# Optimization experiments

Hardware: AMD Instinct MI355X
Metric: run time of the kernel (lower is better)

## Reference

```python
import jax, jax.numpy as jnp
import numpy as np

N = 20000
E = 320000
IN_DIM = 128
HIDDEN = 256
HEADS = 4
HD = HIDDEN // HEADS  # 64 per-head channels in layer 1
OUT_DIM = 128
NEG_SLOPE = 0.2
BN_EPS = 1e-5


def setup_inputs() -> dict:
    key = jax.random.key(0)
    ks = jax.random.split(key, 16)
    inp = {
        "x": jax.random.normal(ks[0], (N, IN_DIM), dtype=jnp.float32),
        "edge_index": jax.random.randint(ks[1], (2, E), 0, N, dtype=jnp.int64),
        # layer 1: GATConv(IN_DIM, HD, heads=HEADS, concat=True)
        "W1": jax.random.normal(ks[2], (IN_DIM, HEADS * HD), dtype=jnp.float32) * (1.0 / np.sqrt(IN_DIM)),
        "att_src1": jax.random.normal(ks[3], (HEADS, HD), dtype=jnp.float32) * 0.1,
        "att_dst1": jax.random.normal(ks[4], (HEADS, HD), dtype=jnp.float32) * 0.1,
        "bias1": jnp.zeros((HEADS * HD,), dtype=jnp.float32),
        "bn1_gamma": jnp.ones((HIDDEN,), dtype=jnp.float32),
        "bn1_beta": jnp.zeros((HIDDEN,), dtype=jnp.float32),
        # layer 2: GATConv(HIDDEN, OUT_DIM, heads=1, concat=False)
        "W2": jax.random.normal(ks[5], (HIDDEN, OUT_DIM), dtype=jnp.float32) * (1.0 / np.sqrt(HIDDEN)),
        "att_src2": jax.random.normal(ks[6], (1, OUT_DIM), dtype=jnp.float32) * 0.1,
        "att_dst2": jax.random.normal(ks[7], (1, OUT_DIM), dtype=jnp.float32) * 0.1,
        "bias2": jnp.zeros((OUT_DIM,), dtype=jnp.float32),
        "bn2_gamma": jnp.ones((OUT_DIM,), dtype=jnp.float32),
        "bn2_beta": jnp.zeros((OUT_DIM,), dtype=jnp.float32),
    }
    return inp


def _gat_conv(x, src, dst, W, a_src, a_dst, bias, heads, concat):
    """PyG GATConv with add_self_loops=True (self-loops already in src/dst)."""
    n = x.shape[0]
    hd = W.shape[1] // heads
    h = (x @ W).reshape(n, heads, hd)                     # [N, H, hd]
    alpha_s = jnp.einsum('nhd,hd->nh', h, a_src)          # [N, H]
    alpha_d = jnp.einsum('nhd,hd->nh', h, a_dst)          # [N, H]
    e = alpha_s[src] + alpha_d[dst]                       # [Etot, H]
    e = jnp.where(e > 0, e, NEG_SLOPE * e)                # leaky_relu
    # edge-softmax over incoming edges of each destination node
    m = jax.ops.segment_max(e, dst, num_segments=n)       # [N, H]
    ex = jnp.exp(e - m[dst])
    denom = jax.ops.segment_sum(ex, dst, num_segments=n)  # [N, H]
    alpha = ex / (denom[dst] + 1e-16)                     # [Etot, H]
    msg = h[src] * alpha[..., None]                       # [Etot, H, hd]
    out = jax.ops.segment_sum(msg, dst, num_segments=n)   # [N, H, hd]
    if concat:
        out = out.reshape(n, heads * hd)
    else:
        out = out.mean(axis=1)
    return out + bias


def _batch_norm(x, gamma, beta):
    mean = x.mean(axis=0)
    var = ((x - mean) ** 2).mean(axis=0)  # biased, training-mode BN
    return (x - mean) * jax.lax.rsqrt(var + BN_EPS) * gamma + beta


def reference(x, edge_index, W1, att_src1, att_dst1, bias1, bn1_gamma, bn1_beta,
              W2, att_src2, att_dst2, bias2, bn2_gamma, bn2_beta):
    n = x.shape[0]
    loop = jnp.arange(n, dtype=edge_index.dtype)
    src = jnp.concatenate([edge_index[0], loop])  # add self-loops (PyG default)
    dst = jnp.concatenate([edge_index[1], loop])

    h = _gat_conv(x, src, dst, W1, att_src1, att_dst1, bias1, HEADS, True)
    h = _batch_norm(h, bn1_gamma, bn1_beta)
    h = jax.nn.elu(h)

    h = _gat_conv(h, src, dst, W2, att_src2, att_dst2, bias2, 1, False)
    h = _batch_norm(h, bn2_gamma, bn2_beta)
    return h
```

## Files before the change

kernel.cpp:

```cpp
#include <hip/hip_runtime.h>
#include <type_traits>

constexpr int N_N  = 20000;
constexpr int N_E  = 320000;
constexpr int N_ET = N_E + N_N;
constexpr int IN_D = 128;
constexpr int HID  = 256;
constexpr int H1   = 4;
constexpr int OUTD = 128;
constexpr float SLOPE = 0.2f;
constexpr float BNEPS = 1e-5f;
constexpr int NPART = 32;

typedef unsigned short u16;
typedef float f32x4 __attribute__((ext_vector_type(4)));
typedef short bf16x8 __attribute__((ext_vector_type(8)));

__device__ __forceinline__ float bf2f(u16 u) { return __uint_as_float((unsigned)u << 16); }
__device__ __forceinline__ u16 f2bf(float f) {
  unsigned u = __float_as_uint(f);
  unsigned r = u + 0x7FFFu + ((u >> 16) & 1u);
  return (u16)(r >> 16);
}

__global__ __launch_bounds__(256) void prep_k(const int* __restrict__ ei,
                                              const float* __restrict__ W1,
                                              const float* __restrict__ W2,
                                              u16* __restrict__ wp1,
                                              u16* __restrict__ wp2,
                                              int* __restrict__ cnt) {
  const int i = blockIdx.x * 256 + threadIdx.x;
  if (i < IN_D * HID) {
    const int n = i >> 7, k = i & 127;
    wp1[i] = f2bf(W1[(size_t)k * HID + n]);
  }
  if (i < HID * OUTD) {
    const int n = i >> 8, k = i & 255;
    wp2[i] = f2bf(W2[(size_t)k * OUTD + n]);
  }
  if (i < N_ET) {
    const int dst = (i < N_E) ? ei[N_E + i] : (i - N_E);
    atomicAdd(&cnt[dst], 1);
  }
}

__global__ __launch_bounds__(1024) void scan_k(const int* __restrict__ cnt,
                                               int* __restrict__ rowptr,
                                               int* __restrict__ wcur) {
  __shared__ int wsum[17];
  const int tid = threadIdx.x, lane = tid & 63, wv = tid >> 6;
  constexpr int CHK = 20;
  const int base = tid * CHK;
  int c[CHK];
  int s = 0;
#pragma unroll
  for (int j = 0; j < CHK; ++j) {
    const int idx = base + j;
    c[j] = (idx < N_N) ? cnt[idx] : 0;
    s += c[j];
  }
  const int own = s;
#pragma unroll
  for (int off = 1; off < 64; off <<= 1) {
    const int v = __shfl_up(s, off, 64);
    if (lane >= off) s += v;
  }
  if (lane == 63) wsum[wv] = s;
  __syncthreads();
  if (tid == 0) {
    int run = 0;
#pragma unroll
    for (int i = 0; i < 16; ++i) { const int t = wsum[i]; wsum[i] = run; run += t; }
    wsum[16] = run;
  }
  __syncthreads();
  int run = wsum[wv] + (s - own);
#pragma unroll
  for (int j = 0; j < CHK; ++j) {
    const int idx = base + j;
    if (idx < N_N) {
      rowptr[idx] = run;
      wcur[idx]   = run;
      run += c[j];
    }
  }
  if (tid == 0) rowptr[N_N] = wsum[16];
}

constexpr int GB1 = N_N / 16;
__global__ __launch_bounds__(256) void sg_k(const float* __restrict__ x,
                                            const u16* __restrict__ wp,
                                            const float* __restrict__ asrc,
                                            const float* __restrict__ adst,
                                            u16* __restrict__ h,
                                            float* __restrict__ as_,
                                            float* __restrict__ ad_,
                                            const int* __restrict__ ei,
                                            int* __restrict__ wcur,
                                            int* __restrict__ col) {
  const int tid = threadIdx.x;
  if (blockIdx.x >= GB1) {
    const int i = (blockIdx.x - GB1) * 256 + tid;
    if (i >= N_ET) return;
    int s, dst;
    if (i < N_E) { s = ei[i]; dst = ei[N_E + i]; } else { s = dst = i - N_E; }
    const int pos = atomicAdd(&wcur[dst], 1);
    col[pos] = s;
    return;
  }
  const int wv = tid >> 6, lane = tid & 63;
  const int q = lane >> 4, t = lane & 15;
  const int m0 = blockIdx.x * 16;
  const int n0 = wv * 64;
  f32x4 acc[4] = {};
#pragma unroll
  for (int kb = 0; kb < 4; ++kb) {
    const int k0 = kb * 32 + q * 8;
    const float4 x0 = *(const float4*)(x + (size_t)(m0 + t) * 128 + k0);
    const float4 x1 = *(const float4*)(x + (size_t)(m0 + t) * 128 + k0 + 4);
    bf16x8 a;
    a[0] = (short)f2bf(x0.x); a[1] = (short)f2bf(x0.y);
    a[2] = (short)f2bf(x0.z); a[3] = (short)f2bf(x0.w);
    a[4] = (short)f2bf(x1.x); a[5] = (short)f2bf(x1.y);
    a[6] = (short)f2bf(x1.z); a[7] = (short)f2bf(x1.w);
#pragma unroll
    for (int nt = 0; nt < 4; ++nt) {
      const int n = n0 + nt * 16 + t;
      const bf16x8 b = *(const bf16x8*)(wp + (size_t)n * 128 + k0);
      acc[nt] = __builtin_amdgcn_mfma_f32_16x16x32_bf16(a, b, acc[nt], 0, 0, 0);
    }
  }
  float ps[4] = {0.f, 0.f, 0.f, 0.f}, pd[4] = {0.f, 0.f, 0.f, 0.f};
#pragma unroll
  for (int nt = 0; nt < 4; ++nt) {
    const int coln = n0 + nt * 16 + t;
    const float a_s = asrc[coln], a_d = adst[coln];
#pragma unroll
    for (int r = 0; r < 4; ++r) {
      const float d = acc[nt][r];
      h[(size_t)(m0 + q * 4 + r) * 256 + coln] = f2bf(d);
      ps[r] += d * a_s;
      pd[r] += d * a_d;
    }
  }
#pragma unroll
  for (int off = 1; off < 16; off <<= 1)
#pragma unroll
    for (int r = 0; r < 4; ++r) {
      ps[r] += __shfl_xor(ps[r], off, 64);
      pd[r] += __shfl_xor(pd[r], off, 64);
    }
  if (t == 0) {
#pragma unroll
    for (int r = 0; r < 4; ++r) {
      const int row = m0 + q * 4 + r;
      as_[(size_t)row * 4 + wv] = ps[r];
      ad_[(size_t)row * 4 + wv] = pd[r];
    }
  }
}

__global__ __launch_bounds__(256) void gat_agg1_k(const int* __restrict__ rowptr,
                                                  const int* __restrict__ col,
                                                  const u16* __restrict__ h,
                                                  const float* __restrict__ as_,
                                                  const float* __restrict__ ad_,
                                                  u16* __restrict__ out,
                                                  float* __restrict__ accp) {
  __shared__ __align__(16) float s_w[4][64][4];
  __shared__ __align__(16) float st_s[4][256], st_q[4][256];
  const int tid = threadIdx.x;
  const int wv = tid >> 6, lane = tid & 63;
  const int n = blockIdx.x * 4 + wv;
  const int beg = rowptr[n], end = rowptr[n + 1];
  const int c0 = lane * 4;
  const int hl = lane >> 4;
  const float4 adv = *(const float4*)(ad_ + (size_t)n * 4);

  float a0 = 0.f, a1 = 0.f, a2 = 0.f, a3 = 0.f, smh = 0.f;

  for (int j0 = beg; j0 < end; j0 += 64) {
    const int cnt = min(64, end - j0);
    const int j = j0 + lane;
    const int sl = col[(j < end) ? j : beg];

    ushort4 gA[8];
#pragma unroll
    for (int u = 0; u < 8; ++u) {
      const int sv = __shfl(sl, u, 64);
      gA[u] = *(const ushort4*)(h + (size_t)sv * 256 + c0);
    }

    const float4 av = *(const float4*)(as_ + (size_t)sl * 4);
    float e0 = av.x + adv.x; e0 = e0 > 0.f ? e0 : SLOPE * e0;
    float e1 = av.y + adv.y; e1 = e1 > 0.f ? e1 : SLOPE * e1;
    float e2 = av.z + adv.z; e2 = e2 > 0.f ? e2 : SLOPE * e2;
    float e3 = av.w + adv.w; e3 = e3 > 0.f ? e3 : SLOPE * e3;
    const bool valid = j < end;
    float4 w4;
    w4.x = valid ? __expf(e0) : 0.f;
    w4.y = valid ? __expf(e1) : 0.f;
    w4.z = valid ? __expf(e2) : 0.f;
    w4.w = valid ? __expf(e3) : 0.f;
    *(float4*)(&s_w[wv][lane][0]) = w4;

    const int rounds = (cnt + 7) >> 3;
    for (int r = 0; r < rounds; ++r) {
      ushort4 gB[8];
      if (r + 1 < rounds) {
        const int nb = (r + 1) * 8;
#pragma unroll
        for (int u = 0; u < 8; ++u) {
          const int sv = __shfl(sl, nb + u, 64);
          gB[u] = *(const ushort4*)(h + (size_t)sv * 256 + c0);
        }
      }
      const int rb = r * 8;
#pragma unroll
      for (int u = 0; u < 8; ++u) {
        const float w = s_w[wv][rb + u][hl];
        smh += w;
        a0 = fmaf(w, bf2f(gA[u].x), a0);
        a1 = fmaf(w, bf2f(gA[u].y), a1);
        a2 = fmaf(w, bf2f(gA[u].z), a2);
        a3 = fmaf(w, bf2f(gA[u].w), a3);
      }
      if (r + 1 < rounds) {
#pragma unroll
        for (int u = 0; u < 8; ++u) gA[u] = gB[u];
      }
    }
  }

  const float rr = 1.f / (smh + 1e-16f);
  const float v0 = a0 * rr, v1 = a1 * rr, v2 = a2 * rr, v3 = a3 * rr;
  ushort4 o;
  o.x = f2bf(v0); o.y = f2bf(v1); o.z = f2bf(v2); o.w = f2bf(v3);
  *(ushort4*)(out + (size_t)n * 256 + c0) = o;

  float4 sv4, qv4;
  sv4.x = v0; sv4.y = v1; sv4.z = v2; sv4.w = v3;
  qv4.x = v0 * v0; qv4.y = v1 * v1; qv4.z = v2 * v2; qv4.w = v3 * v3;
  *(float4*)(&st_s[wv][c0]) = sv4;
  *(float4*)(&st_q[wv][c0]) = qv4;
  __syncthreads();
  {
    const int c = tid;
    const float s = st_s[0][c] + st_s[1][c] + st_s[2][c] + st_s[3][c];
    const float q = st_q[0][c] + st_q[1][c] + st_q[2][c] + st_q[3][c];
    float* dst = accp + (size_t)(blockIdx.x & (NPART - 1)) * 512;
    atomicAdd(&dst[c], s);
    atomicAdd(&dst[256 + c], q);
  }
}

__global__ __launch_bounds__(256) void gat_agg2_k(const int* __restrict__ rowptr,
                                                  const int* __restrict__ col,
                                                  const u16* __restrict__ h,
                                                  const float* __restrict__ as_,
                                                  const float* __restrict__ ad_,
                                                  u16* __restrict__ out,
                                                  float* __restrict__ accp) {
  __shared__ __align__(16) float st_s[4][128], st_q[4][128];
  const int tid = threadIdx.x;
  const int wv = tid >> 6, lane = tid & 63;
  const int n = blockIdx.x * 4 + wv;
  const int beg = rowptr[n], end = rowptr[n + 1];
  const int eh = lane >> 5;
  const int cl = (lane & 31) * 4;
  const float adv = ad_[n];

  float a0 = 0.f, a1 = 0.f, a2 = 0.f, a3 = 0.f, smh = 0.f;

  for (int j0 = beg; j0 < end; j0 += 64) {
    const int cnt = min(64, end - j0);
    const int j = j0 + lane;
    const int sl = col[(j < end) ? j : beg];
    float e = as_[sl] + adv;
    e = e > 0.f ? e : SLOPE * e;
    const float ew = (j < end) ? __expf(e) : 0.f;

    const int rounds = (cnt + 15) >> 4;
    ushort4 gA[8];
#pragma unroll
    for (int u = 0; u < 8; ++u) {
      const int es = u * 2 + eh;
      const int sv = __shfl(sl, es, 64);
      gA[u] = *(const ushort4*)(h + (size_t)sv * 128 + cl);
    }
    for (int r = 0; r < rounds; ++r) {
      ushort4 gB[8];
      if (r + 1 < rounds) {
        const int nb = (r + 1) * 16;
#pragma unroll
        for (int u = 0; u < 8; ++u) {
          const int es = nb + u * 2 + eh;
          const int sv = __shfl(sl, es, 64);
          gB[u] = *(const ushort4*)(h + (size_t)sv * 128 + cl);
        }
      }
      const int rb = r * 16;
#pragma unroll
      for (int u = 0; u < 8; ++u) {
        const float w = __shfl(ew, rb + u * 2 + eh, 64);
        smh += w;
        a0 = fmaf(w, bf2f(gA[u].x), a0);
        a1 = fmaf(w, bf2f(gA[u].y), a1);
        a2 = fmaf(w, bf2f(gA[u].z), a2);
        a3 = fmaf(w, bf2f(gA[u].w), a3);
      }
      if (r + 1 < rounds) {
#pragma unroll
        for (int u = 0; u < 8; ++u) gA[u] = gB[u];
      }
    }
  }

  a0 += __shfl_xor(a0, 32, 64);
  a1 += __shfl_xor(a1, 32, 64);
  a2 += __shfl_xor(a2, 32, 64);
  a3 += __shfl_xor(a3, 32, 64);
  smh += __shfl_xor(smh, 32, 64);

  const float rr = 1.f / (smh + 1e-16f);
  const float v0 = a0 * rr, v1 = a1 * rr, v2 = a2 * rr, v3 = a3 * rr;
  if (lane < 32) {
    ushort4 o;
    o.x = f2bf(v0); o.y = f2bf(v1); o.z = f2bf(v2); o.w = f2bf(v3);
    *(ushort4*)(out + (size_t)n * 128 + cl) = o;
    float4 sv4, qv4;
    sv4.x = v0; sv4.y = v1; sv4.z = v2; sv4.w = v3;
    qv4.x = v0 * v0; qv4.y = v1 * v1; qv4.z = v2 * v2; qv4.w = v3 * v3;
    *(float4*)(&st_s[wv][cl]) = sv4;
    *(float4*)(&st_q[wv][cl]) = qv4;
  }
  __syncthreads();
  if (tid < 128) {
    const int c = tid;
    const float s = st_s[0][c] + st_s[1][c] + st_s[2][c] + st_s[3][c];
    const float q = st_q[0][c] + st_q[1][c] + st_q[2][c] + st_q[3][c];
    float* dst = accp + (size_t)(blockIdx.x & (NPART - 1)) * 256;
    atomicAdd(&dst[c], s);
    atomicAdd(&dst[128 + c], q);
  }
}

__global__ __launch_bounds__(256) void gemm2_mfma_k(const u16* __restrict__ hin,
                                                    const float* __restrict__ accp,
                                                    const float* __restrict__ g1,
                                                    const float* __restrict__ b1,
                                                    const u16* __restrict__ wp,
                                                    const float* __restrict__ asrc,
                                                    const float* __restrict__ adst,
                                                    u16* __restrict__ h2,
                                                    float* __restrict__ as_,
                                                    float* __restrict__ ad_) {
  __shared__ float scsh[512];
  __shared__ float red[2][32][2];
  const int tid = threadIdx.x;
  {
    float s = 0.f, q = 0.f;
#pragma unroll
    for (int p = 0; p < NPART; ++p) {
      s += accp[(size_t)p * 512 + tid];
      q += accp[(size_t)p * 512 + 256 + tid];
    }
    const float mean = s * (1.f / N_N);
    const float var  = q * (1.f / N_N) - mean * mean;
    const float inv  = rsqrtf(var + BNEPS);
    const float sc   = g1[tid] * inv;
    scsh[tid]       = sc;
    scsh[256 + tid] = b1[tid] - mean * sc;
  }
  __syncthreads();
  const int wv = tid >> 6, lane = tid & 63;
  const int q = lane >> 4, t = lane & 15;
  const int mh = wv >> 1, nh = wv & 1;
  const int m0 = blockIdx.x * 32 + mh * 16;
  const int n0 = nh * 64;
  f32x4 acc[4] = {};
#pragma unroll
  for (int kb = 0; kb < 8; ++kb) {
    const int k0 = kb * 32 + q * 8;
    const ushort4 u0 = *(const ushort4*)(hin + (size_t)(m0 + t) * 256 + k0);
    const ushort4 u1 = *(const ushort4*)(hin + (size_t)(m0 + t) * 256 + k0 + 4);
    const float4 sc0 = *(const float4*)(scsh + k0);
    const float4 sc1 = *(const float4*)(scsh + k0 + 4);
    const float4 sh0 = *(const float4*)(scsh + 256 + k0);
    const float4 sh1 = *(const float4*)(scsh + 256 + k0 + 4);
    float v[8];
    v[0] = bf2f(u0.x) * sc0.x + sh0.x;
    v[1] = bf2f(u0.y) * sc0.y + sh0.y;
    v[2] = bf2f(u0.z) * sc0.z + sh0.z;
    v[3] = bf2f(u0.w) * sc0.w + sh0.w;
    v[4] = bf2f(u1.x) * sc1.x + sh1.x;
    v[5] = bf2f(u1.y) * sc1.y + sh1.y;
    v[6] = bf2f(u1.z) * sc1.z + sh1.z;
    v[7] = bf2f(u1.w) * sc1.w + sh1.w;
    bf16x8 a;
#pragma unroll
    for (int j = 0; j < 8; ++j) {
      const float e = v[j] > 0.f ? v[j] : __expf(v[j]) - 1.f;
      a[j] = (short)f2bf(e);
    }
#pragma unroll
    for (int nt = 0; nt < 4; ++nt) {
      const int n = n0 + nt * 16 + t;
      const bf16x8 b = *(const bf16x8*)(wp + (size_t)n * 256 + k0);
      acc[nt] = __builtin_amdgcn_mfma_f32_16x16x32_bf16(a, b, acc[nt], 0, 0, 0);
    }
  }
  float ps[4] = {0.f, 0.f, 0.f, 0.f}, pd[4] = {0.f, 0.f, 0.f, 0.f};
#pragma unroll
  for (int nt = 0; nt < 4; ++nt) {
    const int coln = n0 + nt * 16 + t;
    const float a_s = asrc[coln], a_d = adst[coln];
#pragma unroll
    for (int r = 0; r < 4; ++r) {
      const float d = acc[nt][r];
      h2[(size_t)(m0 + q * 4 + r) * 128 + coln] = f2bf(d);
      ps[r] += d * a_s;
      pd[r] += d * a_d;
    }
  }
#pragma unroll
  for (int off = 1; off < 16; off <<= 1)
#pragma unroll
    for (int r = 0; r < 4; ++r) {
      ps[r] += __shfl_xor(ps[r], off, 64);
      pd[r] += __shfl_xor(pd[r], off, 64);
    }
  if (t == 0) {
#pragma unroll
    for (int r = 0; r < 4; ++r) {
      red[0][mh * 16 + q * 4 + r][nh] = ps[r];
      red[1][mh * 16 + q * 4 + r][nh] = pd[r];
    }
  }
  __syncthreads();
  if (tid < 32) {
    as_[(size_t)blockIdx.x * 32 + tid] = red[0][tid][0] + red[0][tid][1];
    ad_[(size_t)blockIdx.x * 32 + tid] = red[1][tid][0] + red[1][tid][1];
  }
}

__global__ __launch_bounds__(256) void apply_k(const u16* __restrict__ X,
                                               const float* __restrict__ accp,
                                               const float* __restrict__ gamma,
                                               const float* __restrict__ beta,
                                               float* __restrict__ Y) {
  __shared__ float s_sc[128], s_sh[128];
  const int tid = threadIdx.x;
  if (tid < 128) {
    float s = 0.f, q = 0.f;
#pragma unroll
    for (int p = 0; p < NPART; ++p) {
      s += accp[(size_t)p * 256 + tid];
      q += accp[(size_t)p * 256 + 128 + tid];
    }
    const float mean = s * (1.f / N_N);
    const float var  = q * (1.f / N_N) - mean * mean;
    const float inv  = rsqrtf(var + BNEPS);
    const float sc   = gamma[tid] * inv;
    s_sc[tid] = sc;
    s_sh[tid] = beta[tid] - mean * sc;
  }
  __syncthreads();
  constexpr size_t TOT = (size_t)N_N * OUTD;
  for (size_t i = ((size_t)blockIdx.x * 256 + tid) * 4; i < TOT;
       i += (size_t)gridDim.x * 256 * 4) {
    const ushort4 u = *(const ushort4*)(X + i);
    const int c = (int)(i & 127);
    float4 o;
    o.x = bf2f(u.x) * s_sc[c]     + s_sh[c];
    o.y = bf2f(u.y) * s_sc[c + 1] + s_sh[c + 1];
    o.z = bf2f(u.z) * s_sc[c + 2] + s_sh[c + 2];
    o.w = bf2f(u.w) * s_sc[c + 3] + s_sh[c + 3];
    *(float4*)(Y + i) = o;
  }
}

constexpr size_t OFF_WP1  = 0;
constexpr size_t OFF_WP2  = OFF_WP1  + (size_t)IN_D * HID / 2;
constexpr size_t OFF_H1   = OFF_WP2  + (size_t)HID * OUTD / 2;
constexpr size_t OFF_OUT1 = OFF_H1   + (size_t)N_N * HID / 2;
constexpr size_t OFF_H2   = OFF_OUT1 + (size_t)N_N * HID / 2;
constexpr size_t OFF_OUT2 = OFF_H2   + (size_t)N_N * OUTD / 2;
constexpr size_t OFF_AS1  = OFF_OUT2 + (size_t)N_N * OUTD / 2;
constexpr size_t OFF_AD1  = OFF_AS1  + (size_t)N_N * H1;
constexpr size_t OFF_AS2  = OFF_AD1  + (size_t)N_N * H1;
constexpr size_t OFF_AD2  = OFF_AS2  + (size_t)N_N;
constexpr size_t OFF_ROWP = OFF_AD2  + (size_t)N_N;
constexpr size_t OFF_COL  = OFF_ROWP + (size_t)(N_N + 1);
constexpr size_t OFF_WCUR = OFF_COL  + (size_t)N_ET;
constexpr size_t OFF_CNT  = OFF_WCUR + (size_t)N_N;
constexpr size_t OFF_ACC1 = OFF_CNT  + (size_t)N_N;
constexpr size_t OFF_ACC2 = OFF_ACC1 + (size_t)NPART * 512;
constexpr size_t OFF_ZEND = OFF_ACC2 + (size_t)NPART * 256;

extern "C" void kernel_launch(void* const* d_in, const int* in_sizes, int n_in,
                              void* d_out, int out_size, void* d_ws, size_t ws_size,
                              hipStream_t stream) {
  const float* x      = (const float*)d_in[0];
  const int*   ei     = (const int*)d_in[1];
  const float* W1     = (const float*)d_in[2];
  const float* asrc1  = (const float*)d_in[3];
  const float* adst1  = (const float*)d_in[4];
  const float* g1     = (const float*)d_in[6];
  const float* b1     = (const float*)d_in[7];
  const float* W2     = (const float*)d_in[8];
  const float* asrc2  = (const float*)d_in[9];
  const float* adst2  = (const float*)d_in[10];
  const float* g2     = (const float*)d_in[12];
  const float* b2     = (const float*)d_in[13];

  float* ws = (float*)d_ws;
  u16*   wp1   = (u16*)(ws + OFF_WP1);
  u16*   wp2   = (u16*)(ws + OFF_WP2);
  u16*   h1    = (u16*)(ws + OFF_H1);
  u16*   out1  = (u16*)(ws + OFF_OUT1);
  u16*   h2    = (u16*)(ws + OFF_H2);
  u16*   out2  = (u16*)(ws + OFF_OUT2);
  float* as1   = ws + OFF_AS1;
  float* ad1   = ws + OFF_AD1;
  float* as2   = ws + OFF_AS2;
  float* ad2   = ws + OFF_AD2;
  int*   rowp  = (int*)(ws + OFF_ROWP);
  int*   col   = (int*)(ws + OFF_COL);
  int*   wcur  = (int*)(ws + OFF_WCUR);
  int*   cnt   = (int*)(ws + OFF_CNT);
  float* acc1p = ws + OFF_ACC1;
  float* acc2p = ws + OFF_ACC2;
  float* outf  = (float*)d_out;

  hipMemsetAsync(cnt, 0, (OFF_ZEND - OFF_CNT) * sizeof(float), stream);

  const int eb = (N_ET + 255) / 256;
  prep_k<<<eb, 256, 0, stream>>>(ei, W1, W2, wp1, wp2, cnt);
  scan_k<<<1, 1024, 0, stream>>>(cnt, rowp, wcur);
  sg_k<<<GB1 + eb, 256, 0, stream>>>(x, wp1, asrc1, adst1, h1, as1, ad1, ei, wcur, col);
  gat_agg1_k<<<N_N / 4, 256, 0, stream>>>(rowp, col, h1, as1, ad1, out1, acc1p);
  gemm2_mfma_k<<<N_N / 32, 256, 0, stream>>>(out1, acc1p, g1, b1, wp2, asrc2, adst2, h2, as2, ad2);
  gat_agg2_k<<<N_N / 4, 256, 0, stream>>>(rowp, col, h2, as2, ad2, out2, acc2p);
  apply_k<<<512, 256, 0, stream>>>(out2, acc2p, g2, b2, outf);
}
```

Before: 235.5 us.

## Spread BN stat atomics over more partitions and finalize BN in dedicated kernels

Raises the number of partial-sum slots for the batch-norm atomics from 32 to 512, which cuts atomic contention in the aggregation kernels. Two small kernels now reduce these partials once and write the scale and shift vectors. Before this, every gemm2 and apply block re-reduced all partials itself. In exchange there are two extra kernel launches and a larger memset of the partial buffers.

After: 242.9 us. +3.1%, slower.

```diff
diff --git a/kernel.cpp b/kernel.cpp
--- a/kernel.cpp
+++ b/kernel.cpp
@@ -10,7 +10,7 @@
 constexpr int OUTD = 128;
 constexpr float SLOPE = 0.2f;
 constexpr float BNEPS = 1e-5f;
-constexpr int NPART = 32;
+constexpr int NPART = 512;
 
 typedef unsigned short u16;
 typedef float f32x4 __attribute__((ext_vector_type(4)));
@@ -254,6 +254,34 @@
   }
 }
 
+__global__ __launch_bounds__(256) void bnfin1_k(const float* __restrict__ accp,
+                                                const float* __restrict__ g,
+                                                const float* __restrict__ b,
+                                                float* __restrict__ bnf) {
+  const int wv = threadIdx.x >> 6, lane = threadIdx.x & 63;
+  const int c = blockIdx.x * 4 + wv;
+  float s = 0.f, q = 0.f;
+#pragma unroll
+  for (int k = 0; k < NPART / 64; ++k) {
+    const int p = k * 64 + lane;
+    s += accp[(size_t)p * 512 + c];
+    q += accp[(size_t)p * 512 + 256 + c];
+  }
+#pragma unroll
+  for (int off = 1; off < 64; off <<= 1) {
+    s += __shfl_xor(s, off, 64);
+    q += __shfl_xor(q, off, 64);
+  }
+  if (lane == 0) {
+    const float mean = s * (1.f / N_N);
+    const float var  = q * (1.f / N_N) - mean * mean;
+    const float inv  = rsqrtf(var + BNEPS);
+    const float sc   = g[c] * inv;
+    bnf[c]       = sc;
+    bnf[256 + c] = b[c] - mean * sc;
+  }
+}
+
 __global__ __launch_bounds__(256) void gat_agg2_k(const int* __restrict__ rowptr,
                                                   const int* __restrict__ col,
                                                   const u16* __restrict__ h,
@@ -345,10 +373,36 @@
   }
 }
 
+__global__ __launch_bounds__(256) void bnfin2_k(const float* __restrict__ accp,
+                                                const float* __restrict__ g,
+                                                const float* __restrict__ b,
+                                                float* __restrict__ bnf) {
+  const int wv = threadIdx.x >> 6, lane = threadIdx.x & 63;
+  const int c = blockIdx.x * 4 + wv;
+  float s = 0.f, q = 0.f;
+#pragma unroll
+  for (int k = 0; k < NPART / 64; ++k) {
+    const int p = k * 64 + lane;
+    s += accp[(size_t)p * 256 + c];
+    q += accp[(size_t)p * 256 + 128 + c];
+  }
+#pragma unroll
+  for (int off = 1; off < 64; off <<= 1) {
+    s += __shfl_xor(s, off, 64);
+    q += __shfl_xor(q, off, 64);
+  }
+  if (lane == 0) {
+    const float mean = s * (1.f / N_N);
+    const float var  = q * (1.f / N_N) - mean * mean;
+    const float inv  = rsqrtf(var + BNEPS);
+    const float sc   = g[c] * inv;
+    bnf[c]       = sc;
+    bnf[128 + c] = b[c] - mean * sc;
+  }
+}
+
 __global__ __launch_bounds__(256) void gemm2_mfma_k(const u16* __restrict__ hin,
-                                                    const float* __restrict__ accp,
-                                                    const float* __restrict__ g1,
-                                                    const float* __restrict__ b1,
+                                                    const float* __restrict__ bnf,
                                                     const u16* __restrict__ wp,
                                                     const float* __restrict__ asrc,
                                                     const float* __restrict__ adst,
@@ -358,20 +412,8 @@
   __shared__ float scsh[512];
   __shared__ float red[2][32][2];
   const int tid = threadIdx.x;
-  {
-    float s = 0.f, q = 0.f;
-#pragma unroll
-    for (int p = 0; p < NPART; ++p) {
-      s += accp[(size_t)p * 512 + tid];
-      q += accp[(size_t)p * 512 + 256 + tid];
-    }
-    const float mean = s * (1.f / N_N);
-    const float var  = q * (1.f / N_N) - mean * mean;
-    const float inv  = rsqrtf(var + BNEPS);
-    const float sc   = g1[tid] * inv;
-    scsh[tid]       = sc;
-    scsh[256 + tid] = b1[tid] - mean * sc;
-  }
+  scsh[tid]       = bnf[tid];
+  scsh[256 + tid] = bnf[256 + tid];
   __syncthreads();
   const int wv = tid >> 6, lane = tid & 63;
   const int q = lane >> 4, t = lane & 15;
@@ -445,25 +487,13 @@
 }
 
 __global__ __launch_bounds__(256) void apply_k(const u16* __restrict__ X,
-                                               const float* __restrict__ accp,
-                                               const float* __restrict__ gamma,
-                                               const float* __restrict__ beta,
+                                               const float* __restrict__ bnf,
                                                float* __restrict__ Y) {
   __shared__ float s_sc[128], s_sh[128];
   const int tid = threadIdx.x;
   if (tid < 128) {
-    float s = 0.f, q = 0.f;
-#pragma unroll
-    for (int p = 0; p < NPART; ++p) {
-      s += accp[(size_t)p * 256 + tid];
-      q += accp[(size_t)p * 256 + 128 + tid];
-    }
-    const float mean = s * (1.f / N_N);
-    const float var  = q * (1.f / N_N) - mean * mean;
-    const float inv  = rsqrtf(var + BNEPS);
-    const float sc   = gamma[tid] * inv;
-    s_sc[tid] = sc;
-    s_sh[tid] = beta[tid] - mean * sc;
+    s_sc[tid] = bnf[tid];
+    s_sh[tid] = bnf[128 + tid];
   }
   __syncthreads();
   constexpr size_t TOT = (size_t)N_N * OUTD;
@@ -497,6 +527,8 @@
 constexpr size_t OFF_ACC1 = OFF_CNT  + (size_t)N_N;
 constexpr size_t OFF_ACC2 = OFF_ACC1 + (size_t)NPART * 512;
 constexpr size_t OFF_ZEND = OFF_ACC2 + (size_t)NPART * 256;
+constexpr size_t OFF_BN1F = OFF_ZEND;
+constexpr size_t OFF_BN2F = OFF_BN1F + 512;
 
 extern "C" void kernel_launch(void* const* d_in, const int* in_sizes, int n_in,
                               void* d_out, int out_size, void* d_ws, size_t ws_size,
@@ -531,6 +563,8 @@
   int*   cnt   = (int*)(ws + OFF_CNT);
   float* acc1p = ws + OFF_ACC1;
   float* acc2p = ws + OFF_ACC2;
+  float* bn1f  = ws + OFF_BN1F;
+  float* bn2f  = ws + OFF_BN2F;
   float* outf  = (float*)d_out;
 
   hipMemsetAsync(cnt, 0, (OFF_ZEND - OFF_CNT) * sizeof(float), stream);
@@ -540,7 +574,9 @@
   scan_k<<<1, 1024, 0, stream>>>(cnt, rowp, wcur);
   sg_k<<<GB1 + eb, 256, 0, stream>>>(x, wp1, asrc1, adst1, h1, as1, ad1, ei, wcur, col);
   gat_agg1_k<<<N_N / 4, 256, 0, stream>>>(rowp, col, h1, as1, ad1, out1, acc1p);
-  gemm2_mfma_k<<<N_N / 32, 256, 0, stream>>>(out1, acc1p, g1, b1, wp2, asrc2, adst2, h2, as2, ad2);
+  bnfin1_k<<<64, 256, 0, stream>>>(acc1p, g1, b1, bn1f);
+  gemm2_mfma_k<<<N_N / 32, 256, 0, stream>>>(out1, bn1f, wp2, asrc2, adst2, h2, as2, ad2);
   gat_agg2_k<<<N_N / 4, 256, 0, stream>>>(rowp, col, h2, as2, ad2, out2, acc2p);
-  apply_k<<<512, 256, 0, stream>>>(out2, acc2p, g2, b2, outf);
-}
+  bnfin2_k<<<32, 256, 0, stream>>>(acc2p, g2, b2, bn2f);
+  apply_k<<<512, 256, 0, stream>>>(out2, acc2p  == acc2p ? bn2f : bn2f, outf);
+}
```
